# Optimization experiments

Measured on AMD Instinct MI355X. Metric: run time of the kernel, lower is better.

The kernel has to match this reference:

```python
import jax, jax.numpy as jnp
import numpy as np

B, T, C, H = 4, 2048, 1024, 16
D = C // H
NEG = -1e9


def setup_inputs() -> dict:
    key = jax.random.key(0)
    ks = jax.random.split(key, 4)
    x = jax.random.normal(ks[0], (B, T, C), dtype=jnp.float32)
    # additive causal mask: 0 on/below diagonal, -1e9 above
    causal = jnp.triu(jnp.full((T, T), NEG, dtype=jnp.float32), k=1)
    mask = causal[None, None, :, :]
    W_attn = jax.random.normal(ks[1], (C, 3 * C), dtype=jnp.float32) * (1.0 / np.sqrt(C))
    b_attn = jnp.zeros((3 * C,), dtype=jnp.float32)
    W_proj = jax.random.normal(ks[2], (C, C), dtype=jnp.float32) * (1.0 / np.sqrt(C))
    b_proj = jnp.zeros((C,), dtype=jnp.float32)
    return {"x": x, "mask": mask, "W_attn": W_attn, "b_attn": b_attn,
            "W_proj": W_proj, "b_proj": b_proj}


def reference(x, mask, W_attn, b_attn, W_proj, b_proj):
    b, t, c = x.shape
    qkv = x @ W_attn + b_attn                      # [b,t,3c]
    q, k, v = jnp.split(qkv, 3, axis=2)
    # [b,h,t,d]
    q = q.reshape(b, t, H, D).transpose(0, 2, 1, 3)
    k = k.reshape(b, t, H, D).transpose(0, 2, 1, 3)
    v = v.reshape(b, t, H, D).transpose(0, 2, 1, 3)
    att = jnp.einsum('bhqd,bhkd->bhqk', q, k) * (1.0 / np.sqrt(D))
    att = att + mask
    att = jax.nn.softmax(att, axis=-1)
    out = jnp.einsum('bhqk,bhkd->bhqd', att, v)    # [b,h,t,d]
    out = out.transpose(0, 2, 1, 3).reshape(b, t, c)
    out = out @ W_proj + b_proj
    return out, k, v
```

## Files before the change

### kernel.cpp

```cpp
#include <hip/hip_runtime.h>
#include <stdint.h>

typedef short  s16x8 __attribute__((ext_vector_type(8)));
typedef ushort u16x8 __attribute__((ext_vector_type(8)));
typedef float  f32x4 __attribute__((ext_vector_type(4)));

constexpr int BB = 4, TT = 2048, CC = 1024, HH = 16, DD = 64;
constexpr int MM = BB * TT;
constexpr int N_QKV = 3 * CC;
constexpr size_t KSEG = (size_t)MM * CC;
constexpr size_t VSEG = 2 * KSEG;

#define SWZ64(row, uoff) ((row) * 64 + ((uoff) ^ (((row) & 7) << 3)))
#define SWZ32(row, uoff) ((row) * 32 + ((uoff) ^ (((row) & 3) << 3)))

__device__ __forceinline__ ushort bf16_rne(float f) {
  uint32_t u = __builtin_bit_cast(uint32_t, f);
  u += 0x7fffu + ((u >> 16) & 1u);
  return (ushort)(u >> 16);
}
__device__ __forceinline__ float bf16_to_f32(ushort h) {
  uint32_t u = ((uint32_t)h) << 16;
  return __builtin_bit_cast(float, u);
}
__device__ __forceinline__ void split_hl(float f, ushort &hi, ushort &lo) {
  hi = bf16_rne(f);
  lo = bf16_rne(f - bf16_to_f32(hi));
}
__device__ __forceinline__ f32x4 mfma16(s16x8 a, s16x8 b, f32x4 c) {
  return __builtin_amdgcn_mfma_f32_16x16x32_bf16(a, b, c, 0, 0, 0);
}

__global__ void k_convert(const float* __restrict__ src, ushort* __restrict__ hi,
                          ushort* __restrict__ lo, int n8) {
  int i = blockIdx.x * blockDim.x + threadIdx.x;
  if (i >= n8) return;
  float4 a = ((const float4*)src)[2 * i];
  float4 b = ((const float4*)src)[2 * i + 1];
  float f[8] = {a.x, a.y, a.z, a.w, b.x, b.y, b.z, b.w};
  u16x8 h, l;
#pragma unroll
  for (int j = 0; j < 8; j++) { ushort hh, ll; split_hl(f[j], hh, ll); h[j] = hh; l[j] = ll; }
  *(u16x8*)(hi + 8 * (size_t)i) = h;
  *(u16x8*)(lo + 8 * (size_t)i) = l;
}

__global__ void k_transpose_split(const float* __restrict__ W, ushort* __restrict__ Th,
                                  ushort* __restrict__ Tl, int K, int N) {
  __shared__ float tile[32][33];
  int nt = blockIdx.x * 32, kt = blockIdx.y * 32;
  int tx = threadIdx.x, ty = threadIdx.y;
#pragma unroll
  for (int i = 0; i < 4; i++)
    tile[ty + i * 8][tx] = W[(size_t)(kt + ty + i * 8) * N + nt + tx];
  __syncthreads();
#pragma unroll
  for (int i = 0; i < 4; i++) {
    int nl = ty + i * 8;
    float f = tile[tx][nl];
    ushort h, l; split_hl(f, h, l);
    size_t o = (size_t)(nt + nl) * K + kt + tx;
    Th[o] = h; Tl[o] = l;
  }
}

template<int MODE>
__global__ __launch_bounds__(256) void k_gemm(
    const ushort* __restrict__ Ah, const ushort* __restrict__ Al,
    const ushort* __restrict__ Bth, const ushort* __restrict__ Btl,
    const float* __restrict__ bias, int K,
    float* __restrict__ outF, ushort* __restrict__ q_hi, ushort* __restrict__ q_lo,
    ushort* __restrict__ kh, ushort* __restrict__ kl,
    ushort* __restrict__ vth, ushort* __restrict__ vtl) {
  __shared__ ushort sAh[128 * 32], sAl[128 * 32], sBh[128 * 32], sBl[128 * 32];
  const int tid = threadIdx.x;
  const int wave = tid >> 6, lane = tid & 63;
  const int wr = wave >> 1, wc = wave & 1;
  const int lr = lane & 15, lg = lane >> 4;
  const int m0 = blockIdx.y * 128, n0 = blockIdx.x * 128;
  const int srow = tid >> 2;
  const int sk = (tid & 3) * 8;

  f32x4 acc[4][4] = {};

  for (int kt = 0; kt < K; kt += 32) {
#pragma unroll
    for (int p = 0; p < 2; p++) {
      int row = srow + p * 64;
      size_t ga = (size_t)(m0 + row) * K + kt + sk;
      size_t gb = (size_t)(n0 + row) * K + kt + sk;
      int d = SWZ32(row, sk);
      *(u16x8*)(sAh + d) = *(const u16x8*)(Ah + ga);
      *(u16x8*)(sAl + d) = *(const u16x8*)(Al + ga);
      *(u16x8*)(sBh + d) = *(const u16x8*)(Bth + gb);
      *(u16x8*)(sBl + d) = *(const u16x8*)(Btl + gb);
    }
    __syncthreads();
    s16x8 fah[4], fal[4], fbh[4], fbl[4];
#pragma unroll
    for (int i = 0; i < 4; i++) {
      int ra = wr * 64 + i * 16 + lr, rb = wc * 64 + i * 16 + lr;
      fah[i] = *(const s16x8*)(sAh + SWZ32(ra, lg * 8));
      fal[i] = *(const s16x8*)(sAl + SWZ32(ra, lg * 8));
      fbh[i] = *(const s16x8*)(sBh + SWZ32(rb, lg * 8));
      fbl[i] = *(const s16x8*)(sBl + SWZ32(rb, lg * 8));
    }
#pragma unroll
    for (int mf = 0; mf < 4; mf++)
#pragma unroll
      for (int nf = 0; nf < 4; nf++) {
        acc[mf][nf] = mfma16(fah[mf], fbh[nf], acc[mf][nf]);
        acc[mf][nf] = mfma16(fah[mf], fbl[nf], acc[mf][nf]);
        acc[mf][nf] = mfma16(fal[mf], fbh[nf], acc[mf][nf]);
      }
    __syncthreads();
  }

#pragma unroll
  for (int mf = 0; mf < 4; mf++) {
#pragma unroll
    for (int nf = 0; nf < 4; nf++) {
      int n = n0 + wc * 64 + nf * 16 + lr;
      float bv = bias[n];
#pragma unroll
      for (int r = 0; r < 4; r++) {
        int m = m0 + wr * 64 + mf * 16 + lg * 4 + r;
        float v = acc[mf][nf][r] + bv;
        if constexpr (MODE == 0) {
          int b = m >> 11, t = m & 2047;
          int seg = n >> 10, nn = n & 1023;
          int h = nn >> 6, d = nn & 63;
          size_t idx = ((size_t)((b * 16 + h) * 2048 + t)) * 64 + d;
          if (seg == 0) {
            ushort hh, ll; split_hl(v * 0.125f, hh, ll);
            q_hi[idx] = hh; q_lo[idx] = ll;
          } else if (seg == 1) {
            outF[KSEG + idx] = v;
            ushort hh, ll; split_hl(v, hh, ll);
            kh[idx] = hh; kl[idx] = ll;
          } else {
            outF[VSEG + idx] = v;
            ushort hh, ll; split_hl(v, hh, ll);
            size_t vidx = ((size_t)((b * 16 + h) * 64 + d)) * 2048 + t;
            vth[vidx] = hh; vtl[vidx] = ll;
          }
        } else {
          outF[(size_t)m * CC + n] = v;
        }
      }
    }
  }
}

__global__ __launch_bounds__(256, 3) void k_attn(
    const ushort* __restrict__ q_hi, const ushort* __restrict__ q_lo,
    const ushort* __restrict__ kh, const ushort* __restrict__ kl,
    const ushort* __restrict__ vth, const ushort* __restrict__ vtl,
    ushort* __restrict__ att_hi, ushort* __restrict__ att_lo) {
  __shared__ ushort sK0[64 * 64], sK1[64 * 64];
  __shared__ ushort sV0[64 * 64], sV1[64 * 64];
  __shared__ ushort sP0[4][16 * 64], sP1[4][16 * 64];
  const int tid = threadIdx.x, wave = tid >> 6, lane = tid & 63;
  const int lr = lane & 15, lg = lane >> 4;
  const int px = blockIdx.x, bh = blockIdx.y;
  const int qa = px, qb = 31 - px;
  const int qrow_a = qa * 64 + wave * 16;
  const int qrow_b = qb * 64 + wave * 16;

  s16x8 fqah[2], fqal[2], fqbh[2], fqbl[2];
  {
    size_t ba = ((size_t)bh * TT + qrow_a + lr) * 64;
    size_t bb = ((size_t)bh * TT + qrow_b + lr) * 64;
#pragma unroll
    for (int ks = 0; ks < 2; ks++) {
      fqah[ks] = *(const s16x8*)(q_hi + ba + ks * 32 + lg * 8);
      fqal[ks] = *(const s16x8*)(q_lo + ba + ks * 32 + lg * 8);
      fqbh[ks] = *(const s16x8*)(q_hi + bb + ks * 32 + lg * 8);
      fqbl[ks] = *(const s16x8*)(q_lo + bb + ks * 32 + lg * 8);
    }
  }
  float mra[4], lra[4], mrb[4], lrb[4];
#pragma unroll
  for (int r = 0; r < 4; r++) { mra[r] = -INFINITY; lra[r] = 0.f; mrb[r] = -INFINITY; lrb[r] = 0.f; }
  f32x4 oa[4] = {}, ob[4] = {};

  auto tile_step = [&](const s16x8* fqh, const s16x8* fql, float* mrun, float* lrun,
                       f32x4* oacc, bool diag) {
    f32x4 sa[4];
#pragma unroll
    for (int nf = 0; nf < 4; nf++) {
      f32x4 a = {};
#pragma unroll
      for (int ks = 0; ks < 2; ks++) {
        int d = SWZ64(nf * 16 + lr, ks * 32 + lg * 8);
        s16x8 kbh = *(const s16x8*)(sK0 + d);
        s16x8 kbl = *(const s16x8*)(sK1 + d);
        a = mfma16(fqh[ks], kbh, a);
        a = mfma16(fqh[ks], kbl, a);
        a = mfma16(fql[ks], kbh, a);
      }
      sa[nf] = a;
    }
    if (diag) {
#pragma unroll
      for (int nf = 0; nf < 4; nf++) {
        int col = nf * 16 + lr;
#pragma unroll
        for (int r = 0; r < 4; r++)
          if (col > wave * 16 + 4 * lg + r) sa[nf][r] = -1e9f;
      }
    }
    float mx[4];
#pragma unroll
    for (int r = 0; r < 4; r++) {
      float m = fmaxf(fmaxf(sa[0][r], sa[1][r]), fmaxf(sa[2][r], sa[3][r]));
      m = fmaxf(m, __shfl_xor(m, 1));
      m = fmaxf(m, __shfl_xor(m, 2));
      m = fmaxf(m, __shfl_xor(m, 4));
      m = fmaxf(m, __shfl_xor(m, 8));
      mx[r] = m;
    }
    int grow = 0;
#pragma unroll
    for (int r = 0; r < 4; r++) grow |= (mx[r] > mrun[r] + 8.0f);
    if (__any(grow)) {
#pragma unroll
      for (int r = 0; r < 4; r++) {
        float mnew = fmaxf(mrun[r], mx[r]);
        float fr = __expf(mrun[r] - mnew);
        mrun[r] = mnew;
        lrun[r] *= fr;
#pragma unroll
        for (int df = 0; df < 4; df++) oacc[df][r] *= fr;
      }
    }
    float rs[4] = {0.f, 0.f, 0.f, 0.f};
    ushort* Pb0 = sP0[wave];
    ushort* Pb1 = sP1[wave];
#pragma unroll
    for (int nf = 0; nf < 4; nf++) {
#pragma unroll
      for (int r = 0; r < 4; r++) {
        float p = __expf(sa[nf][r] - mrun[r]);
        rs[r] += p;
        ushort h, l; split_hl(p, h, l);
        int d = SWZ64(4 * lg + r, nf * 16 + lr);
        Pb0[d] = h; Pb1[d] = l;
      }
    }
#pragma unroll
    for (int r = 0; r < 4; r++) {
      float s = rs[r];
      s += __shfl_xor(s, 1); s += __shfl_xor(s, 2);
      s += __shfl_xor(s, 4); s += __shfl_xor(s, 8);
      lrun[r] += s;
    }
#pragma unroll
    for (int ks = 0; ks < 2; ks++) {
      int dp = SWZ64(lr, ks * 32 + lg * 8);
      s16x8 ph = *(const s16x8*)(Pb0 + dp);
      s16x8 pl = *(const s16x8*)(Pb1 + dp);
#pragma unroll
      for (int df = 0; df < 4; df++) {
        int dv = SWZ64(df * 16 + lr, ks * 32 + lg * 8);
        s16x8 bvh = *(const s16x8*)(sV0 + dv);
        s16x8 bvl = *(const s16x8*)(sV1 + dv);
        oacc[df] = mfma16(ph, bvh, oacc[df]);
        oacc[df] = mfma16(ph, bvl, oacc[df]);
        oacc[df] = mfma16(pl, bvh, oacc[df]);
      }
    }
  };

  for (int kt = 0; kt <= qb; kt++) {
#pragma unroll
    for (int it = 0; it < 2; it++) {
      int vv = tid + it * 256;
      int row = vv >> 3, cu = (vv & 7) * 8;
      size_t gk = ((size_t)bh * TT + kt * 64 + row) * 64 + cu;
      size_t gv = ((size_t)bh * 64 + row) * TT + kt * 64 + cu;
      int d = SWZ64(row, cu);
      *(u16x8*)(sK0 + d) = *(const u16x8*)(kh + gk);
      *(u16x8*)(sK1 + d) = *(const u16x8*)(kl + gk);
      *(u16x8*)(sV0 + d) = *(const u16x8*)(vth + gv);
      *(u16x8*)(sV1 + d) = *(const u16x8*)(vtl + gv);
    }
    __syncthreads();
    if (kt <= qa) tile_step(fqah, fqal, mra, lra, oa, kt == qa);
    tile_step(fqbh, fqbl, mrb, lrb, ob, kt == qb);
    __syncthreads();
  }

  const int b = bh >> 4, h = bh & 15;
#pragma unroll
  for (int r = 0; r < 4; r++) {
    float inva = 1.0f / lra[r], invb = 1.0f / lrb[r];
    int ta = qrow_a + 4 * lg + r, tb = qrow_b + 4 * lg + r;
#pragma unroll
    for (int df = 0; df < 4; df++) {
      float va = oa[df][r] * inva, vb = ob[df][r] * invb;
      ushort hh, ll;
      size_t ia = ((size_t)(b * TT + ta)) * CC + h * 64 + df * 16 + lr;
      size_t ib = ((size_t)(b * TT + tb)) * CC + h * 64 + df * 16 + lr;
      split_hl(va, hh, ll); att_hi[ia] = hh; att_lo[ia] = ll;
      split_hl(vb, hh, ll); att_hi[ib] = hh; att_lo[ib] = ll;
    }
  }
}

extern "C" void kernel_launch(void* const* d_in, const int* in_sizes, int n_in,
                              void* d_out, int out_size, void* d_ws, size_t ws_size,
                              hipStream_t stream) {
  const float* x      = (const float*)d_in[0];
  const float* W_attn = (const float*)d_in[2];
  const float* b_attn = (const float*)d_in[3];
  const float* W_proj = (const float*)d_in[4];
  const float* b_proj = (const float*)d_in[5];
  float* out = (float*)d_out;

  char* w = (char*)d_ws;
  ushort* x_hi  = (ushort*)w; w += (size_t)MM * CC * 2;
  ushort* x_lo  = (ushort*)w; w += (size_t)MM * CC * 2;
  ushort* waT_h = (ushort*)w; w += (size_t)N_QKV * CC * 2;
  ushort* waT_l = (ushort*)w; w += (size_t)N_QKV * CC * 2;
  ushort* wpT_h = (ushort*)w; w += (size_t)CC * CC * 2;
  ushort* wpT_l = (ushort*)w; w += (size_t)CC * CC * 2;
  ushort* q_hi  = (ushort*)w; w += (size_t)MM * CC * 2;
  ushort* q_lo  = (ushort*)w; w += (size_t)MM * CC * 2;
  ushort* k_hi  = (ushort*)w; w += (size_t)MM * CC * 2;
  ushort* k_lo  = (ushort*)w; w += (size_t)MM * CC * 2;
  ushort* vT_hi = (ushort*)w; w += (size_t)MM * CC * 2;
  ushort* vT_lo = (ushort*)w; w += (size_t)MM * CC * 2;
  ushort* att_h = x_hi;
  ushort* att_l = x_lo;

  hipLaunchKernelGGL(k_convert, dim3((MM * CC / 8 + 255) / 256), dim3(256), 0, stream,
                     x, x_hi, x_lo, MM * CC / 8);
  hipLaunchKernelGGL(k_transpose_split, dim3(N_QKV / 32, CC / 32), dim3(32, 8), 0, stream,
                     W_attn, waT_h, waT_l, CC, N_QKV);
  hipLaunchKernelGGL(k_transpose_split, dim3(CC / 32, CC / 32), dim3(32, 8), 0, stream,
                     W_proj, wpT_h, wpT_l, CC, CC);
  hipLaunchKernelGGL((k_gemm<0>), dim3(N_QKV / 128, MM / 128), dim3(256), 0, stream,
                     x_hi, x_lo, waT_h, waT_l, b_attn, CC, out, q_hi, q_lo,
                     k_hi, k_lo, vT_hi, vT_lo);
  hipLaunchKernelGGL(k_attn, dim3(16, BB * HH), dim3(256), 0, stream,
                     q_hi, q_lo, k_hi, k_lo, vT_hi, vT_lo, att_h, att_l);
  hipLaunchKernelGGL((k_gemm<1>), dim3(CC / 128, MM / 128), dim3(256), 0, stream,
                     att_h, att_l, wpT_h, wpT_l, b_proj, CC, out,
                     nullptr, nullptr, nullptr, nullptr, nullptr, nullptr);
}
```

Measured before the change: 738.9 us.

## Use direct global-to-LDS loads in GEMM and register-prefetch K/V tiles in attention

The GEMM tile loads now use global_load_lds with 16-byte transfers, so data goes straight into shared memory without a register round trip. The swizzle is applied on the global-address side instead of the LDS side. The attention kernel prefetches the next K/V tile into registers while the current tile is computed, which overlaps global latency with the MFMA work. MFMA sections are wrapped in s_setprio to favour matrix issue. The costs are higher register pressure in attention, and the GEMM depends on the lane-to-LDS mapping of the direct load matching the swizzled fragment reads.

```diff
diff --git a/kernel.cpp b/kernel.cpp
--- a/kernel.cpp
+++ b/kernel.cpp
@@ -29,6 +29,11 @@
 }
 __device__ __forceinline__ f32x4 mfma16(s16x8 a, s16x8 b, f32x4 c) {
   return __builtin_amdgcn_mfma_f32_16x16x32_bf16(a, b, c, 0, 0, 0);
+}
+__device__ __forceinline__ void gload16(const ushort* g, ushort* l) {
+  __builtin_amdgcn_global_load_lds(
+      (const __attribute__((address_space(1))) unsigned int*)g,
+      (__attribute__((address_space(3))) unsigned int*)l, 16, 0, 0);
 }
 
 __global__ void k_convert(const float* __restrict__ src, ushort* __restrict__ hi,
@@ -78,22 +83,21 @@
   const int wr = wave >> 1, wc = wave & 1;
   const int lr = lane & 15, lg = lane >> 4;
   const int m0 = blockIdx.y * 128, n0 = blockIdx.x * 128;
-  const int srow = tid >> 2;
-  const int sk = (tid & 3) * 8;
 
   f32x4 acc[4][4] = {};
 
   for (int kt = 0; kt < K; kt += 32) {
 #pragma unroll
-    for (int p = 0; p < 2; p++) {
-      int row = srow + p * 64;
-      size_t ga = (size_t)(m0 + row) * K + kt + sk;
-      size_t gb = (size_t)(n0 + row) * K + kt + sk;
-      int d = SWZ32(row, sk);
-      *(u16x8*)(sAh + d) = *(const u16x8*)(Ah + ga);
-      *(u16x8*)(sAl + d) = *(const u16x8*)(Al + ga);
-      *(u16x8*)(sBh + d) = *(const u16x8*)(Bth + gb);
-      *(u16x8*)(sBl + d) = *(const u16x8*)(Btl + gb);
+    for (int i = 0; i < 2; i++) {
+      int row = wave * 32 + i * 16 + (lane >> 2);
+      int cu = (((lane & 3) ^ (row & 3)) << 3);
+      int ldsoff = (wave * 32 + i * 16) * 32;
+      size_t ga = (size_t)(m0 + row) * K + kt + cu;
+      size_t gb = (size_t)(n0 + row) * K + kt + cu;
+      gload16(Ah + ga, sAh + ldsoff);
+      gload16(Al + ga, sAl + ldsoff);
+      gload16(Bth + gb, sBh + ldsoff);
+      gload16(Btl + gb, sBl + ldsoff);
     }
     __syncthreads();
     s16x8 fah[4], fal[4], fbh[4], fbl[4];
@@ -184,9 +188,37 @@
   for (int r = 0; r < 4; r++) { mra[r] = -INFINITY; lra[r] = 0.f; mrb[r] = -INFINITY; lrb[r] = 0.f; }
   f32x4 oa[4] = {}, ob[4] = {};
 
+  u16x8 rk0[2], rk1[2], rv0[2], rv1[2];
+  auto issue_loads = [&](int kt) {
+#pragma unroll
+    for (int it = 0; it < 2; it++) {
+      int vv = tid + it * 256;
+      int row = vv >> 3, cu = (vv & 7) * 8;
+      size_t gk = ((size_t)bh * TT + kt * 64 + row) * 64 + cu;
+      size_t gv = ((size_t)bh * 64 + row) * TT + kt * 64 + cu;
+      rk0[it] = *(const u16x8*)(kh + gk);
+      rk1[it] = *(const u16x8*)(kl + gk);
+      rv0[it] = *(const u16x8*)(vth + gv);
+      rv1[it] = *(const u16x8*)(vtl + gv);
+    }
+  };
+  auto write_lds = [&]() {
+#pragma unroll
+    for (int it = 0; it < 2; it++) {
+      int vv = tid + it * 256;
+      int row = vv >> 3, cu = (vv & 7) * 8;
+      int d = SWZ64(row, cu);
+      *(u16x8*)(sK0 + d) = rk0[it];
+      *(u16x8*)(sK1 + d) = rk1[it];
+      *(u16x8*)(sV0 + d) = rv0[it];
+      *(u16x8*)(sV1 + d) = rv1[it];
+    }
+  };
+
   auto tile_step = [&](const s16x8* fqh, const s16x8* fql, float* mrun, float* lrun,
                        f32x4* oacc, bool diag) {
     f32x4 sa[4];
+    __builtin_amdgcn_s_setprio(1);
 #pragma unroll
     for (int nf = 0; nf < 4; nf++) {
       f32x4 a = {};
@@ -201,6 +233,7 @@
       }
       sa[nf] = a;
     }
+    __builtin_amdgcn_s_setprio(0);
     if (diag) {
 #pragma unroll
       for (int nf = 0; nf < 4; nf++) {
@@ -255,6 +288,7 @@
       s += __shfl_xor(s, 4); s += __shfl_xor(s, 8);
       lrun[r] += s;
     }
+    __builtin_amdgcn_s_setprio(1);
 #pragma unroll
     for (int ks = 0; ks < 2; ks++) {
       int dp = SWZ64(lr, ks * 32 + lg * 8);
@@ -270,21 +304,13 @@
         oacc[df] = mfma16(pl, bvh, oacc[df]);
       }
     }
+    __builtin_amdgcn_s_setprio(0);
   };
 
+  issue_loads(0);
   for (int kt = 0; kt <= qb; kt++) {
-#pragma unroll
-    for (int it = 0; it < 2; it++) {
-      int vv = tid + it * 256;
-      int row = vv >> 3, cu = (vv & 7) * 8;
-      size_t gk = ((size_t)bh * TT + kt * 64 + row) * 64 + cu;
-      size_t gv = ((size_t)bh * 64 + row) * TT + kt * 64 + cu;
-      int d = SWZ64(row, cu);
-      *(u16x8*)(sK0 + d) = *(const u16x8*)(kh + gk);
-      *(u16x8*)(sK1 + d) = *(const u16x8*)(kl + gk);
-      *(u16x8*)(sV0 + d) = *(const u16x8*)(vth + gv);
-      *(u16x8*)(sV1 + d) = *(const u16x8*)(vtl + gv);
-    }
+    write_lds();
+    if (kt < qb) issue_loads(kt + 1);
     __syncthreads();
     if (kt <= qa) tile_step(fqah, fqal, mra, lra, oa, kt == qa);
     tile_step(fqbh, fqbl, mrb, lrb, ob, kt == qb);
```

Result: slower. 840.5 us (+13.7%).
